# Performance work log

Hardware: AMD Instinct MI355X
Metric: run time of the kernel (lower is better)

## Reference

```python
import jax, jax.numpy as jnp
import numpy as np

N = 4096        # batch_size per view
D = 256         # embed_dim
TEMPERATURE = 0.1


def setup_inputs() -> dict:
    key = jax.random.key(0)
    k1, k2 = jax.random.split(key)
    return {
        "z_i": jax.random.normal(k1, (N, D), dtype=jnp.float32),
        "z_j": jax.random.normal(k2, (N, D), dtype=jnp.float32),
    }


def reference(z_i, z_j):
    n = z_i.shape[0]
    # L2-normalize each row (CosineSimilarity == dot of normalized vectors)
    zi = z_i * jax.lax.rsqrt(jnp.sum(z_i * z_i, axis=1, keepdims=True))
    zj = z_j * jax.lax.rsqrt(jnp.sum(z_j * z_j, axis=1, keepdims=True))
    r = jnp.concatenate([zj, zi], axis=0)               # [2n, d], order matches torch cat([z_j, z_i])
    S = (r @ r.T) / TEMPERATURE                          # [2n, 2n] normalized GEMM, no O(n^2 d) broadcast

    idx = jnp.arange(2 * n)
    pos_col = (idx + n) % (2 * n)                        # positive partner: diag(+n) / diag(-n)
    pos = S[idx, pos_col]                                # [2n]

    # Faithful mask: the original masks the diagonal AND both full cross blocks,
    # so negatives are same-view off-diagonal entries only. Keep = negatives + positive.
    same_block = (idx[:, None] // n) == (idx[None, :] // n)
    keep = (same_block & (idx[:, None] != idx[None, :])) | (idx[None, :] == pos_col[:, None])

    # CrossEntropy with label 0 and reduction='sum', then / (2n)  ==  mean(logsumexp - pos)
    lse = jax.nn.logsumexp(jnp.where(keep, S, -jnp.inf), axis=1)  # [2n]
    return jnp.mean(lse - pos)
```

## Files before the change

### kernel.cpp

```cpp
#include <hip/hip_runtime.h>
#include <math.h>

#define N_ROWS 4096
#define DIM 256
constexpr float INV_T = 10.0f;

#define NT 32
#define NTILES 528
#define BM 128
#define PSTRIDE 512

typedef __attribute__((ext_vector_type(4))) float floatx4;

typedef __attribute__((address_space(3))) unsigned int lds_uint;
typedef const __attribute__((address_space(1))) unsigned int glb_uint;

__global__ __launch_bounds__(256) void normalize_kernel(
    const float* __restrict__ z_i, const float* __restrict__ z_j,
    unsigned char* __restrict__ R0, unsigned char* __restrict__ R1,
    float* __restrict__ pos, float* __restrict__ out)
{
    if (blockIdx.x == 0 && threadIdx.x == 0) out[0] = 0.0f;

    int wave = threadIdx.x >> 6;
    int lane = threadIdx.x & 63;
    int row = blockIdx.x * 4 + wave;

    float4 a = ((const float4*)(z_i + (size_t)row * DIM))[lane];
    float4 b = ((const float4*)(z_j + (size_t)row * DIM))[lane];

    float ssa = a.x*a.x + a.y*a.y + a.z*a.z + a.w*a.w;
    float ssb = b.x*b.x + b.y*b.y + b.z*b.z + b.w*b.w;
    float dab = a.x*b.x + a.y*b.y + a.z*b.z + a.w*b.w;
    #pragma unroll
    for (int off = 1; off < 64; off <<= 1) {
        ssa += __shfl_xor(ssa, off);
        ssb += __shfl_xor(ssb, off);
        dab += __shfl_xor(dab, off);
    }
    float ra = rsqrtf(ssa);
    float rb = rsqrtf(ssb);

    int va = __builtin_amdgcn_cvt_pk_fp8_f32(a.x * ra, a.y * ra, 0, false);
    va     = __builtin_amdgcn_cvt_pk_fp8_f32(a.z * ra, a.w * ra, va, true);
    int vb = __builtin_amdgcn_cvt_pk_fp8_f32(b.x * rb, b.y * rb, 0, false);
    vb     = __builtin_amdgcn_cvt_pk_fp8_f32(b.z * rb, b.w * rb, vb, true);

    *(int*)(R1 + (size_t)row * DIM + lane * 4) = va;
    *(int*)(R0 + (size_t)row * DIM + lane * 4) = vb;

    if (lane == 0) pos[row] = dab * ra * rb * INV_T;
}

__global__ __launch_bounds__(256) void gemm_sym(
    const unsigned char* __restrict__ R0,
    const unsigned char* __restrict__ R1,
    float* __restrict__ part)
{
    __shared__ unsigned char As[BM * DIM];
    __shared__ unsigned char Bs[BM * DIM];

    int view = blockIdx.y;
    const unsigned char* R = view ? R1 : R0;
    float* P = part + (size_t)(view * NTILES + blockIdx.x) * PSTRIDE;

    int t = blockIdx.x;
    int by = 0;
    while (t >= NT - by) { t -= NT - by; ++by; }
    int bx = by + t;
    int rT = by * BM, cT = bx * BM;

    int tid = threadIdx.x;
    int lane = tid & 63;
    int wave = tid >> 6;
    int wy = wave >> 1, wx = wave & 1;
    int m = lane & 15, q = lane >> 4;

    #pragma unroll
    for (int stp = 0; stp < 8; ++stp) {
        int s = stp * 256 + tid;
        int row = s >> 4, p = s & 15;
        int cg = p ^ (row & 15);
        const unsigned char* ga = R + (size_t)(rT + row) * DIM + cg * 16;
        const unsigned char* gb = R + (size_t)(cT + row) * DIM + cg * 16;
        __builtin_amdgcn_global_load_lds((glb_uint*)ga, (lds_uint*)&As[s * 16], 16, 0, 0);
        __builtin_amdgcn_global_load_lds((glb_uint*)gb, (lds_uint*)&Bs[s * 16], 16, 0, 0);
    }
    __syncthreads();

    floatx4 acc[4][4] = {};

    #pragma unroll
    for (int kk = 0; kk < 8; ++kk) {
        long af[4], bf[4];
        int c = kk * 4 + q;
        int ch = c >> 1, hh = (c & 1) * 8;
        #pragma unroll
        for (int tt = 0; tt < 4; ++tt) {
            int ra = wy * 64 + tt * 16 + m;
            af[tt] = *(const long*)&As[ra * DIM + (ch ^ (ra & 15)) * 16 + hh];
            int rb = wx * 64 + tt * 16 + m;
            bf[tt] = *(const long*)&Bs[rb * DIM + (ch ^ (rb & 15)) * 16 + hh];
        }
        #pragma unroll
        for (int i = 0; i < 4; ++i)
            #pragma unroll
            for (int j = 0; j < 4; ++j)
                acc[i][j] = __builtin_amdgcn_mfma_f32_16x16x32_fp8_fp8(af[i], bf[j], acc[i][j], 0, 0, 0);
    }

    float rs[4][4] = {};
    float cs[4] = {0.f, 0.f, 0.f, 0.f};
    #pragma unroll
    for (int i = 0; i < 4; ++i) {
        #pragma unroll
        for (int j = 0; j < 4; ++j) {
            int gcol = cT + wx * 64 + j * 16 + m;
            #pragma unroll
            for (int r = 0; r < 4; ++r) {
                int grow = rT + wy * 64 + i * 16 + q * 4 + r;
                float e = (grow == gcol) ? 0.0f : __expf(acc[i][j][r] * INV_T);
                rs[i][r] += e;
                cs[j] += e;
            }
        }
    }
    #pragma unroll
    for (int off = 1; off < 16; off <<= 1)
        #pragma unroll
        for (int i = 0; i < 4; ++i)
            #pragma unroll
            for (int r = 0; r < 4; ++r)
                rs[i][r] += __shfl_xor(rs[i][r], off);
    if (m == 0) {
        #pragma unroll
        for (int i = 0; i < 4; ++i) {
            float4 v = make_float4(rs[i][0], rs[i][1], rs[i][2], rs[i][3]);
            *(float4*)&P[wx * 128 + wy * 64 + i * 16 + q * 4] = v;
        }
    }
    #pragma unroll
    for (int off = 16; off < 64; off <<= 1)
        #pragma unroll
        for (int j = 0; j < 4; ++j)
            cs[j] += __shfl_xor(cs[j], off);
    if (q == 0) {
        #pragma unroll
        for (int j = 0; j < 4; ++j)
            P[256 + wy * 128 + wx * 64 + j * 16 + m] = (bx == by) ? 0.0f : cs[j];
    }
}

__global__ __launch_bounds__(256) void finalize_kernel(
    const float* __restrict__ part, const float* __restrict__ pos,
    float* __restrict__ out)
{
    int g = blockIdx.x * 256 + threadIdx.x;
    int v = g >> 12, r = g & (N_ROWS - 1);
    int b = r >> 7, l = r & 127;
    const float* P = part + (size_t)v * NTILES * PSTRIDE;

    float d = 0.f;
    int t0 = b * NT - (b * (b - 1)) / 2;
    for (int k = 0; k < NT - b; ++k) {
        const float* T = P + (size_t)(t0 + k) * PSTRIDE;
        d += T[l] + T[128 + l];
    }
    for (int by = 0; by <= b; ++by) {
        int tb = by * NT - (by * (by - 1)) / 2 + (b - by);
        const float* T = P + (size_t)tb * PSTRIDE;
        d += T[256 + l] + T[384 + l];
    }
    float p = pos[r];
    float s = __logf(d + __expf(p)) - p;
    #pragma unroll
    for (int off = 1; off < 64; off <<= 1) s += __shfl_xor(s, off);
    if ((threadIdx.x & 63) == 0)
        atomicAdd(out, s * (1.0f / (2 * N_ROWS)));
}

extern "C" void kernel_launch(void* const* d_in, const int* in_sizes, int n_in,
                              void* d_out, int out_size, void* d_ws, size_t ws_size,
                              hipStream_t stream) {
    const float* z_i = (const float*)d_in[0];
    const float* z_j = (const float*)d_in[1];
    char* ws = (char*)d_ws;
    unsigned char* R0 = (unsigned char*)ws;
    unsigned char* R1 = (unsigned char*)(ws + (1u << 20));
    float* pos  = (float*)(ws + (2u << 20));
    float* part = (float*)(ws + (2u << 20) + (64u << 10));

    normalize_kernel<<<N_ROWS / 4, 256, 0, stream>>>(z_i, z_j, R0, R1, pos,
                                                     (float*)d_out);
    dim3 grid(NTILES, 2);
    gemm_sym<<<grid, 256, 0, stream>>>(R0, R1, part);
    finalize_kernel<<<2 * N_ROWS / 256, 256, 0, stream>>>(part, pos, (float*)d_out);
}
```

Measured before the change: 88.01 us.

## Fuse finalize reduction into GEMM via last-blocks ticket counter

```diff
diff --git a/kernel.cpp b/kernel.cpp
--- a/kernel.cpp
+++ b/kernel.cpp
@@ -7,20 +7,24 @@
 
 #define NT 32
 #define NTILES 528
+#define TOTAL_TILES (2 * NTILES)
+#define FINALIZERS 32
 #define BM 128
 #define PSTRIDE 512
 
 typedef __attribute__((ext_vector_type(4))) float floatx4;
-
 typedef __attribute__((address_space(3))) unsigned int lds_uint;
 typedef const __attribute__((address_space(1))) unsigned int glb_uint;
+
+#define ST_DEV(p, v) __hip_atomic_store((p), (v), __ATOMIC_RELAXED, __HIP_MEMORY_SCOPE_AGENT)
+#define LD_DEV(p)    __hip_atomic_load((p), __ATOMIC_RELAXED, __HIP_MEMORY_SCOPE_AGENT)
 
 __global__ __launch_bounds__(256) void normalize_kernel(
     const float* __restrict__ z_i, const float* __restrict__ z_j,
     unsigned char* __restrict__ R0, unsigned char* __restrict__ R1,
-    float* __restrict__ pos, float* __restrict__ out)
+    float* __restrict__ pos, int* __restrict__ counter, float* __restrict__ out)
 {
-    if (blockIdx.x == 0 && threadIdx.x == 0) out[0] = 0.0f;
+    if (blockIdx.x == 0 && threadIdx.x == 0) { out[0] = 0.0f; *counter = 0; }
 
     int wave = threadIdx.x >> 6;
     int lane = threadIdx.x & 63;
@@ -55,7 +59,10 @@
 __global__ __launch_bounds__(256) void gemm_sym(
     const unsigned char* __restrict__ R0,
     const unsigned char* __restrict__ R1,
-    float* __restrict__ part)
+    float* __restrict__ part,
+    const float* __restrict__ pos,
+    int* __restrict__ counter,
+    float* __restrict__ out)
 {
     __shared__ unsigned char As[BM * DIM];
     __shared__ unsigned char Bs[BM * DIM];
@@ -89,18 +96,17 @@
     __syncthreads();
 
     floatx4 acc[4][4] = {};
-
     #pragma unroll
     for (int kk = 0; kk < 8; ++kk) {
         long af[4], bf[4];
         int c = kk * 4 + q;
         int ch = c >> 1, hh = (c & 1) * 8;
         #pragma unroll
-        for (int tt = 0; tt < 4; ++tt) {
-            int ra = wy * 64 + tt * 16 + m;
-            af[tt] = *(const long*)&As[ra * DIM + (ch ^ (ra & 15)) * 16 + hh];
-            int rb = wx * 64 + tt * 16 + m;
-            bf[tt] = *(const long*)&Bs[rb * DIM + (ch ^ (rb & 15)) * 16 + hh];
+        for (int tr = 0; tr < 4; ++tr) {
+            int ra = wy * 64 + tr * 16 + m;
+            af[tr] = *(const long*)&As[ra * DIM + (ch ^ (ra & 15)) * 16 + hh];
+            int rb = wx * 64 + tr * 16 + m;
+            bf[tr] = *(const long*)&Bs[rb * DIM + (ch ^ (rb & 15)) * 16 + hh];
         }
         #pragma unroll
         for (int i = 0; i < 4; ++i)
@@ -112,7 +118,7 @@
     float rs[4][4] = {};
     float cs[4] = {0.f, 0.f, 0.f, 0.f};
     #pragma unroll
-    for (int i = 0; i < 4; ++i) {
+    for (int i = 0; i < 4; ++i)
         #pragma unroll
         for (int j = 0; j < 4; ++j) {
             int gcol = cT + wx * 64 + j * 16 + m;
@@ -124,7 +130,6 @@
                 cs[j] += e;
             }
         }
-    }
     #pragma unroll
     for (int off = 1; off < 16; off <<= 1)
         #pragma unroll
@@ -134,10 +139,10 @@
                 rs[i][r] += __shfl_xor(rs[i][r], off);
     if (m == 0) {
         #pragma unroll
-        for (int i = 0; i < 4; ++i) {
-            float4 v = make_float4(rs[i][0], rs[i][1], rs[i][2], rs[i][3]);
-            *(float4*)&P[wx * 128 + wy * 64 + i * 16 + q * 4] = v;
-        }
+        for (int i = 0; i < 4; ++i)
+            #pragma unroll
+            for (int r = 0; r < 4; ++r)
+                ST_DEV(&P[wx * 128 + wy * 64 + i * 16 + q * 4 + r], rs[i][r]);
     }
     #pragma unroll
     for (int off = 16; off < 64; off <<= 1)
@@ -147,36 +152,50 @@
     if (q == 0) {
         #pragma unroll
         for (int j = 0; j < 4; ++j)
-            P[256 + wy * 128 + wx * 64 + j * 16 + m] = (bx == by) ? 0.0f : cs[j];
-    }
-}
-
-__global__ __launch_bounds__(256) void finalize_kernel(
-    const float* __restrict__ part, const float* __restrict__ pos,
-    float* __restrict__ out)
-{
-    int g = blockIdx.x * 256 + threadIdx.x;
+            ST_DEV(&P[256 + wy * 128 + wx * 64 + j * 16 + m], (bx == by) ? 0.0f : cs[j]);
+    }
+
+    asm volatile("s_waitcnt vmcnt(0)" ::: "memory");
+    __syncthreads();
+    int* ticket_s = (int*)As;
+    float* red = (float*)As + 2;
+    if (tid == 0)
+        *ticket_s = __hip_atomic_fetch_add(counter, 1, __ATOMIC_RELAXED, __HIP_MEMORY_SCOPE_AGENT);
+    __syncthreads();
+    int ticket = *ticket_s;
+    if (ticket < TOTAL_TILES - FINALIZERS) return;
+
+    if (tid == 0) {
+        while (LD_DEV(counter) < TOTAL_TILES) __builtin_amdgcn_s_sleep(2);
+    }
+    __syncthreads();
+
+    int slice = ticket - (TOTAL_TILES - FINALIZERS);
+    int g = slice * 256 + tid;
     int v = g >> 12, r = g & (N_ROWS - 1);
     int b = r >> 7, l = r & 127;
-    const float* P = part + (size_t)v * NTILES * PSTRIDE;
+    const float* Pv = part + (size_t)v * NTILES * PSTRIDE;
 
     float d = 0.f;
     int t0 = b * NT - (b * (b - 1)) / 2;
     for (int k = 0; k < NT - b; ++k) {
-        const float* T = P + (size_t)(t0 + k) * PSTRIDE;
+        const float* T = Pv + (size_t)(t0 + k) * PSTRIDE;
         d += T[l] + T[128 + l];
     }
-    for (int by = 0; by <= b; ++by) {
-        int tb = by * NT - (by * (by - 1)) / 2 + (b - by);
-        const float* T = P + (size_t)tb * PSTRIDE;
+    for (int by2 = 0; by2 <= b; ++by2) {
+        int tb = by2 * NT - (by2 * (by2 - 1)) / 2 + (b - by2);
+        const float* T = Pv + (size_t)tb * PSTRIDE;
         d += T[256 + l] + T[384 + l];
     }
     float p = pos[r];
     float s = __logf(d + __expf(p)) - p;
     #pragma unroll
     for (int off = 1; off < 64; off <<= 1) s += __shfl_xor(s, off);
-    if ((threadIdx.x & 63) == 0)
-        atomicAdd(out, s * (1.0f / (2 * N_ROWS)));
+    if (lane == 0) red[wave] = s;
+    __syncthreads();
+    if (tid == 0)
+        __hip_atomic_fetch_add(out, (red[0] + red[1] + red[2] + red[3]) * (1.0f / (2 * N_ROWS)),
+                               __ATOMIC_RELAXED, __HIP_MEMORY_SCOPE_AGENT);
 }
 
 extern "C" void kernel_launch(void* const* d_in, const int* in_sizes, int n_in,
@@ -189,10 +208,10 @@
     unsigned char* R1 = (unsigned char*)(ws + (1u << 20));
     float* pos  = (float*)(ws + (2u << 20));
     float* part = (float*)(ws + (2u << 20) + (64u << 10));
+    int* counter = (int*)(ws + (5u << 20));
 
     normalize_kernel<<<N_ROWS / 4, 256, 0, stream>>>(z_i, z_j, R0, R1, pos,
-                                                     (float*)d_out);
+                                                     counter, (float*)d_out);
     dim3 grid(NTILES, 2);
-    gemm_sym<<<grid, 256, 0, stream>>>(R0, R1, part);
-    finalize_kernel<<<2 * N_ROWS / 256, 256, 0, stream>>>(part, pos, (float*)d_out);
+    gemm_sym<<<grid, 256, 0, stream>>>(R0, R1, part, pos, counter, (float*)d_out);
 }
```

Result: slower. 95.43 us (+8.4%).

## Make symmetric GEMM persistent and prefetch next tile during exp epilogue

Applied to the files above, without the earlier changes.

```diff
diff --git a/kernel.cpp b/kernel.cpp
--- a/kernel.cpp
+++ b/kernel.cpp
@@ -7,11 +7,12 @@
 
 #define NT 32
 #define NTILES 528
+#define TOTAL_TILES (2 * NTILES)
+#define GRID_BLOCKS 512
 #define BM 128
 #define PSTRIDE 512
 
 typedef __attribute__((ext_vector_type(4))) float floatx4;
-
 typedef __attribute__((address_space(3))) unsigned int lds_uint;
 typedef const __attribute__((address_space(1))) unsigned int glb_uint;
 
@@ -60,94 +61,115 @@
     __shared__ unsigned char As[BM * DIM];
     __shared__ unsigned char Bs[BM * DIM];
 
-    int view = blockIdx.y;
-    const unsigned char* R = view ? R1 : R0;
-    float* P = part + (size_t)(view * NTILES + blockIdx.x) * PSTRIDE;
-
-    int t = blockIdx.x;
-    int by = 0;
-    while (t >= NT - by) { t -= NT - by; ++by; }
-    int bx = by + t;
-    int rT = by * BM, cT = bx * BM;
-
     int tid = threadIdx.x;
     int lane = tid & 63;
     int wave = tid >> 6;
     int wy = wave >> 1, wx = wave & 1;
     int m = lane & 15, q = lane >> 4;
 
-    #pragma unroll
-    for (int stp = 0; stp < 8; ++stp) {
-        int s = stp * 256 + tid;
-        int row = s >> 4, p = s & 15;
-        int cg = p ^ (row & 15);
-        const unsigned char* ga = R + (size_t)(rT + row) * DIM + cg * 16;
-        const unsigned char* gb = R + (size_t)(cT + row) * DIM + cg * 16;
-        __builtin_amdgcn_global_load_lds((glb_uint*)ga, (lds_uint*)&As[s * 16], 16, 0, 0);
-        __builtin_amdgcn_global_load_lds((glb_uint*)gb, (lds_uint*)&Bs[s * 16], 16, 0, 0);
-    }
-    __syncthreads();
-
-    floatx4 acc[4][4] = {};
-
-    #pragma unroll
-    for (int kk = 0; kk < 8; ++kk) {
-        long af[4], bf[4];
-        int c = kk * 4 + q;
-        int ch = c >> 1, hh = (c & 1) * 8;
-        #pragma unroll
-        for (int tt = 0; tt < 4; ++tt) {
-            int ra = wy * 64 + tt * 16 + m;
-            af[tt] = *(const long*)&As[ra * DIM + (ch ^ (ra & 15)) * 16 + hh];
-            int rb = wx * 64 + tt * 16 + m;
-            bf[tt] = *(const long*)&Bs[rb * DIM + (ch ^ (rb & 15)) * 16 + hh];
-        }
+    auto decode = [&](int tt, int& view, int& by, int& bx) {
+        view = (tt >= NTILES) ? 1 : 0;
+        int t = tt - view * NTILES;
+        by = 0;
+        while (t >= NT - by) { t -= NT - by; ++by; }
+        bx = by + t;
+    };
+    auto stage = [&](const unsigned char* R, int rT, int cT) {
+        #pragma unroll
+        for (int stp = 0; stp < 8; ++stp) {
+            int s = stp * 256 + tid;
+            int row = s >> 4, p = s & 15;
+            int cg = p ^ (row & 15);
+            const unsigned char* ga = R + (size_t)(rT + row) * DIM + cg * 16;
+            const unsigned char* gb = R + (size_t)(cT + row) * DIM + cg * 16;
+            __builtin_amdgcn_global_load_lds((glb_uint*)ga, (lds_uint*)&As[s * 16], 16, 0, 0);
+            __builtin_amdgcn_global_load_lds((glb_uint*)gb, (lds_uint*)&Bs[s * 16], 16, 0, 0);
+        }
+    };
+
+    int tt = blockIdx.x;
+    if (tt >= TOTAL_TILES) return;
+    int view, by, bx;
+    decode(tt, view, by, bx);
+    stage(view ? R1 : R0, by * BM, bx * BM);
+
+    for (;;) {
+        __syncthreads();
+
+        floatx4 acc[4][4] = {};
+        #pragma unroll
+        for (int kk = 0; kk < 8; ++kk) {
+            long af[4], bf[4];
+            int c = kk * 4 + q;
+            int ch = c >> 1, hh = (c & 1) * 8;
+            #pragma unroll
+            for (int tr = 0; tr < 4; ++tr) {
+                int ra = wy * 64 + tr * 16 + m;
+                af[tr] = *(const long*)&As[ra * DIM + (ch ^ (ra & 15)) * 16 + hh];
+                int rb = wx * 64 + tr * 16 + m;
+                bf[tr] = *(const long*)&Bs[rb * DIM + (ch ^ (rb & 15)) * 16 + hh];
+            }
+            #pragma unroll
+            for (int i = 0; i < 4; ++i)
+                #pragma unroll
+                for (int j = 0; j < 4; ++j)
+                    acc[i][j] = __builtin_amdgcn_mfma_f32_16x16x32_fp8_fp8(af[i], bf[j], acc[i][j], 0, 0, 0);
+        }
+
+        __syncthreads();
+
+        int crT = by * BM, ccT = bx * BM;
+        int cdiag = (bx == by);
+        float* P = part + (size_t)tt * PSTRIDE;
+
+        tt += GRID_BLOCKS;
+        bool more = (tt < TOTAL_TILES);
+        if (more) {
+            decode(tt, view, by, bx);
+            stage(view ? R1 : R0, by * BM, bx * BM);
+        }
+
+        float rs[4][4] = {};
+        float cs[4] = {0.f, 0.f, 0.f, 0.f};
         #pragma unroll
         for (int i = 0; i < 4; ++i)
             #pragma unroll
+            for (int j = 0; j < 4; ++j) {
+                int gcol = ccT + wx * 64 + j * 16 + m;
+                #pragma unroll
+                for (int r = 0; r < 4; ++r) {
+                    int grow = crT + wy * 64 + i * 16 + q * 4 + r;
+                    float e = (grow == gcol) ? 0.0f : __expf(acc[i][j][r] * INV_T);
+                    rs[i][r] += e;
+                    cs[j] += e;
+                }
+            }
+        #pragma unroll
+        for (int off = 1; off < 16; off <<= 1)
+            #pragma unroll
+            for (int i = 0; i < 4; ++i)
+                #pragma unroll
+                for (int r = 0; r < 4; ++r)
+                    rs[i][r] += __shfl_xor(rs[i][r], off);
+        if (m == 0) {
+            #pragma unroll
+            for (int i = 0; i < 4; ++i) {
+                float4 v = make_float4(rs[i][0], rs[i][1], rs[i][2], rs[i][3]);
+                *(float4*)&P[wx * 128 + wy * 64 + i * 16 + q * 4] = v;
+            }
+        }
+        #pragma unroll
+        for (int off = 16; off < 64; off <<= 1)
+            #pragma unroll
             for (int j = 0; j < 4; ++j)
-                acc[i][j] = __builtin_amdgcn_mfma_f32_16x16x32_fp8_fp8(af[i], bf[j], acc[i][j], 0, 0, 0);
-    }
-
-    float rs[4][4] = {};
-    float cs[4] = {0.f, 0.f, 0.f, 0.f};
-    #pragma unroll
-    for (int i = 0; i < 4; ++i) {
-        #pragma unroll
-        for (int j = 0; j < 4; ++j) {
-            int gcol = cT + wx * 64 + j * 16 + m;
-            #pragma unroll
-            for (int r = 0; r < 4; ++r) {
-                int grow = rT + wy * 64 + i * 16 + q * 4 + r;
-                float e = (grow == gcol) ? 0.0f : __expf(acc[i][j][r] * INV_T);
-                rs[i][r] += e;
-                cs[j] += e;
-            }
-        }
-    }
-    #pragma unroll
-    for (int off = 1; off < 16; off <<= 1)
-        #pragma unroll
-        for (int i = 0; i < 4; ++i)
-            #pragma unroll
-            for (int r = 0; r < 4; ++r)
-                rs[i][r] += __shfl_xor(rs[i][r], off);
-    if (m == 0) {
-        #pragma unroll
-        for (int i = 0; i < 4; ++i) {
-            float4 v = make_float4(rs[i][0], rs[i][1], rs[i][2], rs[i][3]);
-            *(float4*)&P[wx * 128 + wy * 64 + i * 16 + q * 4] = v;
-        }
-    }
-    #pragma unroll
-    for (int off = 16; off < 64; off <<= 1)
-        #pragma unroll
-        for (int j = 0; j < 4; ++j)
-            cs[j] += __shfl_xor(cs[j], off);
-    if (q == 0) {
-        #pragma unroll
-        for (int j = 0; j < 4; ++j)
-            P[256 + wy * 128 + wx * 64 + j * 16 + m] = (bx == by) ? 0.0f : cs[j];
+                cs[j] += __shfl_xor(cs[j], off);
+        if (q == 0) {
+            #pragma unroll
+            for (int j = 0; j < 4; ++j)
+                P[256 + wy * 128 + wx * 64 + j * 16 + m] = cdiag ? 0.0f : cs[j];
+        }
+
+        if (!more) break;
     }
 }
 
@@ -192,7 +214,6 @@
 
     normalize_kernel<<<N_ROWS / 4, 256, 0, stream>>>(z_i, z_j, R0, R1, pos,
                                                      (float*)d_out);
-    dim3 grid(NTILES, 2);
-    gemm_sym<<<grid, 256, 0, stream>>>(R0, R1, part);
+    gemm_sym<<<GRID_BLOCKS, 256, 0, stream>>>(R0, R1, part);
     finalize_kernel<<<2 * N_ROWS / 256, 256, 0, stream>>>(part, pos, (float*)d_out);
 }
```

Result: no change. 88.70 us (+0.8%).

## Drop in-kernel shuffle reductions and store unreduced partials for finalize

Applied to the files above, without the earlier changes.

```diff
diff --git a/kernel.cpp b/kernel.cpp
--- a/kernel.cpp
+++ b/kernel.cpp
@@ -8,10 +8,9 @@
 #define NT 32
 #define NTILES 528
 #define BM 128
-#define PSTRIDE 512
+#define PSTRIDE 5120
 
 typedef __attribute__((ext_vector_type(4))) float floatx4;
-
 typedef __attribute__((address_space(3))) unsigned int lds_uint;
 typedef const __attribute__((address_space(1))) unsigned int glb_uint;
 
@@ -89,18 +88,17 @@
     __syncthreads();
 
     floatx4 acc[4][4] = {};
-
     #pragma unroll
     for (int kk = 0; kk < 8; ++kk) {
         long af[4], bf[4];
         int c = kk * 4 + q;
         int ch = c >> 1, hh = (c & 1) * 8;
         #pragma unroll
-        for (int tt = 0; tt < 4; ++tt) {
-            int ra = wy * 64 + tt * 16 + m;
-            af[tt] = *(const long*)&As[ra * DIM + (ch ^ (ra & 15)) * 16 + hh];
-            int rb = wx * 64 + tt * 16 + m;
-            bf[tt] = *(const long*)&Bs[rb * DIM + (ch ^ (rb & 15)) * 16 + hh];
+        for (int tr = 0; tr < 4; ++tr) {
+            int ra = wy * 64 + tr * 16 + m;
+            af[tr] = *(const long*)&As[ra * DIM + (ch ^ (ra & 15)) * 16 + hh];
+            int rb = wx * 64 + tr * 16 + m;
+            bf[tr] = *(const long*)&Bs[rb * DIM + (ch ^ (rb & 15)) * 16 + hh];
         }
         #pragma unroll
         for (int i = 0; i < 4; ++i)
@@ -112,7 +110,7 @@
     float rs[4][4] = {};
     float cs[4] = {0.f, 0.f, 0.f, 0.f};
     #pragma unroll
-    for (int i = 0; i < 4; ++i) {
+    for (int i = 0; i < 4; ++i)
         #pragma unroll
         for (int j = 0; j < 4; ++j) {
             int gcol = cT + wx * 64 + j * 16 + m;
@@ -124,31 +122,15 @@
                 cs[j] += e;
             }
         }
-    }
     #pragma unroll
-    for (int off = 1; off < 16; off <<= 1)
+    for (int i = 0; i < 4; ++i)
         #pragma unroll
-        for (int i = 0; i < 4; ++i)
-            #pragma unroll
-            for (int r = 0; r < 4; ++r)
-                rs[i][r] += __shfl_xor(rs[i][r], off);
-    if (m == 0) {
-        #pragma unroll
-        for (int i = 0; i < 4; ++i) {
-            float4 v = make_float4(rs[i][0], rs[i][1], rs[i][2], rs[i][3]);
-            *(float4*)&P[wx * 128 + wy * 64 + i * 16 + q * 4] = v;
-        }
-    }
+        for (int r = 0; r < 4; ++r)
+            P[(wy * 64 + i * 16 + q * 4 + r) * 32 + wx * 16 + m] = rs[i][r];
+    int dz = (bx == by);
     #pragma unroll
-    for (int off = 16; off < 64; off <<= 1)
-        #pragma unroll
-        for (int j = 0; j < 4; ++j)
-            cs[j] += __shfl_xor(cs[j], off);
-    if (q == 0) {
-        #pragma unroll
-        for (int j = 0; j < 4; ++j)
-            P[256 + wy * 128 + wx * 64 + j * 16 + m] = (bx == by) ? 0.0f : cs[j];
-    }
+    for (int j = 0; j < 4; ++j)
+        P[4096 + (wx * 64 + j * 16 + m) * 8 + wy * 4 + q] = dz ? 0.0f : cs[j];
 }
 
 __global__ __launch_bounds__(256) void finalize_kernel(
@@ -156,25 +138,38 @@
     float* __restrict__ out)
 {
     int g = blockIdx.x * 256 + threadIdx.x;
-    int v = g >> 12, r = g & (N_ROWS - 1);
+    int row = g >> 2, sl = g & 3;
+    int v = row >> 12, r = row & (N_ROWS - 1);
     int b = r >> 7, l = r & 127;
-    const float* P = part + (size_t)v * NTILES * PSTRIDE;
+    const float* Pv = part + (size_t)v * NTILES * PSTRIDE;
 
     float d = 0.f;
     int t0 = b * NT - (b * (b - 1)) / 2;
-    for (int k = 0; k < NT - b; ++k) {
-        const float* T = P + (size_t)(t0 + k) * PSTRIDE;
-        d += T[l] + T[128 + l];
+    for (int k = sl; k < NT - b; k += 4) {
+        const float* T = Pv + (size_t)(t0 + k) * PSTRIDE + l * 32;
+        #pragma unroll
+        for (int x = 0; x < 8; ++x) {
+            float4 vv = ((const float4*)T)[x];
+            d += vv.x + vv.y + vv.z + vv.w;
+        }
     }
-    for (int by = 0; by <= b; ++by) {
-        int tb = by * NT - (by * (by - 1)) / 2 + (b - by);
-        const float* T = P + (size_t)tb * PSTRIDE;
-        d += T[256 + l] + T[384 + l];
+    for (int by2 = sl; by2 <= b; by2 += 4) {
+        int tb = by2 * NT - (by2 * (by2 - 1)) / 2 + (b - by2);
+        const float* T = Pv + (size_t)tb * PSTRIDE + 4096 + l * 8;
+        #pragma unroll
+        for (int x = 0; x < 2; ++x) {
+            float4 vv = ((const float4*)T)[x];
+            d += vv.x + vv.y + vv.z + vv.w;
+        }
     }
+    d += __shfl_xor(d, 1);
+    d += __shfl_xor(d, 2);
     float p = pos[r];
-    float s = __logf(d + __expf(p)) - p;
+    float s = (sl == 0) ? (__logf(d + __expf(p)) - p) : 0.0f;
     #pragma unroll
-    for (int off = 1; off < 64; off <<= 1) s += __shfl_xor(s, off);
+    for (int off = 4; off < 64; off <<= 1) s += __shfl_xor(s, off);
+    s += __shfl_xor(s, 1);
+    s += __shfl_xor(s, 2);
     if ((threadIdx.x & 63) == 0)
         atomicAdd(out, s * (1.0f / (2 * N_ROWS)));
 }
@@ -194,5 +189,5 @@
                                                      (float*)d_out);
     dim3 grid(NTILES, 2);
     gemm_sym<<<grid, 256, 0, stream>>>(R0, R1, part);
-    finalize_kernel<<<2 * N_ROWS / 256, 256, 0, stream>>>(part, pos, (float*)d_out);
+    finalize_kernel<<<4 * 2 * N_ROWS / 256, 256, 0, stream>>>(part, pos, (float*)d_out);
 }
```

Measured after the change: 91.41 us. 3.9% more time.
